# Kernel tuning notes

Measured on AMD Instinct MI355X. Metric: run time of the kernel, lower is better.

The kernel has to match this reference:

```python
import jax, jax.numpy as jnp
import numpy as np

NUM_EMB = 8192
EMB_DIM = 512
SPAN = 8            # max_span == fixed_segment_size
COMMIT = 0.25
BOUND_W = 0.01


def setup_inputs() -> dict:
    key = jax.random.key(0)
    k_x, k_e, k_w = jax.random.split(key, 3)
    B, T, D = 16, 8192, EMB_DIM
    x = jax.random.normal(k_x, (B, T, D), dtype=jnp.float32)
    emb = jax.random.normal(k_e, (NUM_EMB, D), dtype=jnp.float32) * 0.02
    Wb = jax.random.normal(k_w, (D, 1), dtype=jnp.float32) * 0.02
    bb = jnp.zeros((1,), dtype=jnp.float32)
    return {"x": x, "emb": emb, "Wb": Wb, "bb": bb}


def reference(x, emb, Wb, bb):
    # Eval-mode forward of AdaptiveTemporalVQ (no gumbel sampling, no EMA update).
    B, T, D = x.shape
    # boundary predictor: Linear(D, 1) -> squeeze
    boundary_logits = (x @ Wb)[..., 0] + bb[0]                      # [B, T]
    boundaries = (jax.nn.sigmoid(boundary_logits) > 0.5).astype(x.dtype)

    num_segments = (T + SPAN - 1) // SPAN
    pad = num_segments * SPAN - T
    x_p = jnp.pad(x, ((0, 0), (0, pad), (0, 0))) if pad > 0 else x
    # temporal mean pooling over fixed segments
    pooled = x_p.reshape(B, num_segments, SPAN, D).mean(axis=2)      # [B, S, D]

    # --- VectorQuantizer ---
    flat = pooled.reshape(-1, D)                                     # [N, D]
    dist = (jnp.sum(flat ** 2, axis=1, keepdims=True)
            + jnp.sum(emb ** 2, axis=1)
            - 2.0 * flat @ emb.T)                                    # [N, K]
    idx = jnp.argmin(dist, axis=1)                                   # [N]
    quantized = emb[idx].reshape(B, num_segments, D)                 # codebook gather

    e_latent_loss = jnp.mean((jax.lax.stop_gradient(quantized) - pooled) ** 2)
    vq_loss = COMMIT * e_latent_loss
    # straight-through estimator
    q_st = pooled + jax.lax.stop_gradient(quantized - pooled)

    # expand each segment code back over its SPAN timesteps
    q_exp = jnp.broadcast_to(q_st[:, :, None, :], (B, num_segments, SPAN, D))
    quantized_out = q_exp.reshape(B, num_segments * SPAN, D)[:, :T, :]
    idx_seg = idx.reshape(B, num_segments)
    idx_out = jnp.broadcast_to(idx_seg[:, :, None], (B, num_segments, SPAN))
    idx_out = idx_out.reshape(B, num_segments * SPAN)[:, :T]

    target_rate = jnp.float32(1.0 / SPAN)
    boundary_loss = (boundaries.mean() - target_rate) ** 2
    total_loss = vq_loss + BOUND_W * boundary_loss
    return quantized_out, total_loss, idx_out, boundaries
```

## Files before the change

### kernel.cpp

```cpp
#include <hip/hip_runtime.h>

#define B_    16
#define T_    8192
#define D_    512
#define K_    8192
#define S_    1024
#define N_    16384
#define NBT   131072

#define LOSS_OFF 67108864
#define IDX_OFF  67108865
#define BND_OFF  67239937

typedef __bf16 bf16x8 __attribute__((ext_vector_type(8)));
typedef float  f32x4  __attribute__((ext_vector_type(4)));

__device__ __forceinline__ unsigned int fsort(float f){
  unsigned int u = __float_as_uint(f);
  return (u & 0x80000000u) ? ~u : (u | 0x80000000u);
}
__device__ __forceinline__ float funsort(unsigned int su){
  unsigned int u = (su & 0x80000000u) ? (su ^ 0x80000000u) : ~su;
  return __uint_as_float(u);
}
__device__ __forceinline__ unsigned short f2bf(float f){
  unsigned int u = __float_as_uint(f);
  return (unsigned short)((u + 0x7fffu + ((u >> 16) & 1u)) >> 16);
}
__device__ __forceinline__ void gload16(const void* g, void* l){
  __builtin_amdgcn_global_load_lds((const __attribute__((address_space(1))) void*)g,
                                   (__attribute__((address_space(3))) void*)l, 16, 0, 0);
}

__global__ void k_init(int* cnt){
  if(threadIdx.x == 0 && blockIdx.x == 0) *cnt = 0;
}

__global__ void k_embnorm(const float4* __restrict__ emb4, float* __restrict__ enorm,
                          unsigned short* __restrict__ embh){
  const int wid  = (blockIdx.x * blockDim.x + threadIdx.x) >> 6;
  const int lane = threadIdx.x & 63;
  float4 a = emb4[wid * 128 + (lane << 1)];
  float4 b = emb4[wid * 128 + (lane << 1) + 1];
  float s = a.x*a.x + a.y*a.y + a.z*a.z + a.w*a.w
          + b.x*b.x + b.y*b.y + b.z*b.z + b.w*b.w;
  #pragma unroll
  for(int off = 32; off; off >>= 1) s += __shfl_xor(s, off);
  if(lane == 0) enorm[wid] = s;
  unsigned short* dst = embh + ((size_t)wid << 9) + (lane << 3);
  *(ushort4*)(dst)     = make_ushort4(f2bf(a.x), f2bf(a.y), f2bf(a.z), f2bf(a.w));
  *(ushort4*)(dst + 4) = make_ushort4(f2bf(b.x), f2bf(b.y), f2bf(b.z), f2bf(b.w));
}

__global__ void k_boundary(const float4* __restrict__ x4, const float4* __restrict__ wb4,
                           const float* __restrict__ bb, float* __restrict__ bnd,
                           int* __restrict__ cnt){
  const int lane = threadIdx.x & 63, wv = threadIdx.x >> 6;
  const int wg = (blockIdx.x << 2) + wv;
  const float4 w0 = wb4[lane << 1], w1 = wb4[(lane << 1) + 1];
  const double bbv = (double)bb[0];
  int c = 0;
  const int rbase = wg << 5;
  for(int r = 0; r < 32; r++){
    const int row = rbase + r;
    float4 a = x4[row * 128 + (lane << 1)];
    float4 b = x4[row * 128 + (lane << 1) + 1];
    double s = (double)a.x*w0.x + (double)a.y*w0.y + (double)a.z*w0.z + (double)a.w*w0.w
             + (double)b.x*w1.x + (double)b.y*w1.y + (double)b.z*w1.z + (double)b.w*w1.w;
    #pragma unroll
    for(int off = 32; off; off >>= 1) s += __shfl_xor(s, off);
    const bool f = (s + bbv) > 0.0;
    if(lane == 0){ bnd[row] = f ? 1.0f : 0.0f; c += (int)f; }
  }
  __shared__ int sc[4];
  if(lane == 0) sc[wv] = c;
  __syncthreads();
  if(threadIdx.x == 0) atomicAdd(cnt, sc[0] + sc[1] + sc[2] + sc[3]);
}

__global__ void k_pool(const float4* __restrict__ x4, float4* __restrict__ pooled4,
                       unsigned short* __restrict__ pooledh){
  const int u = blockIdx.x * 256 + threadIdx.x;
  const int row = u >> 7, c4 = u & 127;
  const int b = row >> 10, s = row & 1023;
  const float4* src = x4 + ((size_t)(b * T_ + (s << 3)) * 128 + c4);
  float4 acc = src[0];
  #pragma unroll
  for(int t = 1; t < 8; t++){
    float4 v = src[(size_t)t * 128];
    acc.x += v.x; acc.y += v.y; acc.z += v.z; acc.w += v.w;
  }
  acc.x *= 0.125f; acc.y *= 0.125f; acc.z *= 0.125f; acc.w *= 0.125f;
  pooled4[u] = acc;
  *(ushort4*)(pooledh + ((size_t)u << 2)) =
      make_ushort4(f2bf(acc.x), f2bf(acc.y), f2bf(acc.z), f2bf(acc.w));
}

__launch_bounds__(256, 2)
__global__ void k_distx(const unsigned short* __restrict__ Ah,
                        const unsigned short* __restrict__ Bh,
                        const float* __restrict__ enorm,
                        unsigned int* __restrict__ cand){
  __shared__ __align__(16) unsigned short sA[4096];
  __shared__ __align__(16) unsigned short sB[4096];
  const int tid  = threadIdx.x;
  const int w    = tid >> 6, lane = tid & 63;
  const int wm   = w >> 1,  wn   = w & 1;
  const int c    = lane & 15, q  = lane >> 4;

  const int bid   = blockIdx.x;
  const int st    = bid >> 9;
  const int loc   = bid & 511;
  const int row_t = (st << 3) + (loc & 7);
  const int col_t = loc >> 3;
  const int rowbase = row_t << 7;
  const int colbase = col_t << 7;

  f32x4 acc[4][4];
  #pragma unroll
  for(int i = 0; i < 4; i++)
    #pragma unroll
    for(int j = 0; j < 4; j++) acc[i][j] = (f32x4){0.f, 0.f, 0.f, 0.f};

  const int sr  = lane >> 2;
  const int skc = (lane & 3) << 3;

  const unsigned short* Ap0 = Ah + (size_t)(rowbase + w*32 + sr)      * 512 + skc;
  const unsigned short* Ap1 = Ah + (size_t)(rowbase + w*32 + 16 + sr) * 512 + skc;
  const unsigned short* Bp0 = Bh + (size_t)(colbase + w*32 + sr)      * 512 + skc;
  const unsigned short* Bp1 = Bh + (size_t)(colbase + w*32 + 16 + sr) * 512 + skc;
  unsigned short* lA0 = &sA[(w*32)      * 32];
  unsigned short* lA1 = &sA[(w*32 + 16) * 32];
  unsigned short* lB0 = &sB[(w*32)      * 32];
  unsigned short* lB1 = &sB[(w*32 + 16) * 32];

  for(int kb = 0; kb < 512; kb += 32){
    gload16(Ap0 + kb, lA0);
    gload16(Ap1 + kb, lA1);
    gload16(Bp0 + kb, lB0);
    gload16(Bp1 + kb, lB1);
    __syncthreads();
    bf16x8 af[4], bg[4];
    #pragma unroll
    for(int i = 0; i < 4; i++) af[i] = *(const bf16x8*)&sA[(wm*64 + i*16 + c)*32 + q*8];
    #pragma unroll
    for(int j = 0; j < 4; j++) bg[j] = *(const bf16x8*)&sB[(wn*64 + j*16 + c)*32 + q*8];
    #pragma unroll
    for(int i = 0; i < 4; i++)
      #pragma unroll
      for(int j = 0; j < 4; j++)
        acc[i][j] = __builtin_amdgcn_mfma_f32_16x16x32_bf16(af[i], bg[j], acc[i][j], 0, 0, 0);
    __syncthreads();
  }

  float en[4];
  #pragma unroll
  for(int j = 0; j < 4; j++) en[j] = enorm[colbase + wn*64 + j*16 + c];

  #pragma unroll
  for(int i = 0; i < 4; i++){
    #pragma unroll
    for(int r = 0; r < 4; r++){
      unsigned int k1 = 0xffffffffu, k2 = 0xffffffffu;
      #pragma unroll
      for(int j = 0; j < 4; j++){
        const float d = fmaf(-2.0f, acc[i][j][r], en[j]);
        const unsigned int col = (unsigned int)(colbase + wn*64 + j*16 + c);
        const unsigned int key = (fsort(d) & 0xffffe000u) | col;
        if(key < k1){ k2 = k1; k1 = key; } else if(key < k2){ k2 = key; }
      }
      #pragma unroll
      for(int off = 1; off < 16; off <<= 1){
        const unsigned int o1 = __shfl_xor(k1, off);
        const unsigned int o2 = __shfl_xor(k2, off);
        if(o1 < k1){ k2 = min(k1, o2); k1 = o1; }
        else       { k2 = min(k2, o1); }
      }
      if(c == 0){
        const int row = rowbase + wm*64 + i*16 + (q << 2) + r;
        unsigned int* o = cand + (((size_t)row << 8) + (col_t << 2) + (wn << 1));
        o[0] = k1; o[1] = k2;
      }
    }
  }
}

__launch_bounds__(256)
__global__ void k_fixup(const float* __restrict__ pooled, const float* __restrict__ emb,
                        const unsigned int* __restrict__ cand,
                        int* __restrict__ idxf, double* __restrict__ part){
  const int lane = threadIdx.x & 63, wv = threadIdx.x >> 6;
  const int row = (blockIdx.x << 2) + wv;
  const unsigned int* cr = cand + ((size_t)row << 8);
  unsigned int ks[4];
  ks[0] = cr[lane]; ks[1] = cr[lane + 64]; ks[2] = cr[lane + 128]; ks[3] = cr[lane + 192];
  unsigned int mn = min(min(ks[0], ks[1]), min(ks[2], ks[3]));
  #pragma unroll
  for(int off = 32; off; off >>= 1) mn = min(mn, (unsigned int)__shfl_xor(mn, off));
  const float thr = funsort(mn & 0xffffe000u) + 0.01f;

  double bestd = 1e300; int besti = 0x7fffffff;
  const float4* p4 = (const float4*)(pooled + ((size_t)row << 9));
  const float4 pa = p4[lane << 1], pb = p4[(lane << 1) + 1];
  #pragma unroll
  for(int g = 0; g < 4; g++){
    const bool flag = funsort(ks[g] & 0xffffe000u) <= thr;
    unsigned long long mask = __ballot(flag);
    while(mask){
      const int l = __ffsll(mask) - 1;
      mask &= mask - 1;
      const int code = (int)(__shfl(ks[g], l) & 0x1fffu);
      const float4* e4 = (const float4*)(emb + ((size_t)code << 9));
      const float4 ea = e4[lane << 1], eb = e4[(lane << 1) + 1];
      double s = 0.0, d;
      d = (double)pa.x - ea.x; s += d * d;  d = (double)pa.y - ea.y; s += d * d;
      d = (double)pa.z - ea.z; s += d * d;  d = (double)pa.w - ea.w; s += d * d;
      d = (double)pb.x - eb.x; s += d * d;  d = (double)pb.y - eb.y; s += d * d;
      d = (double)pb.z - eb.z; s += d * d;  d = (double)pb.w - eb.w; s += d * d;
      #pragma unroll
      for(int off = 32; off; off >>= 1) s += __shfl_xor(s, off);
      if(s < bestd || (s == bestd && code < besti)){ bestd = s; besti = code; }
    }
  }
  __shared__ double se[4];
  if(lane == 0){ idxf[row] = besti; se[wv] = bestd; }
  __syncthreads();
  if(threadIdx.x == 0) part[blockIdx.x] = se[0] + se[1] + se[2] + se[3];
}

__global__ void k_loss(const double* __restrict__ part, const int* __restrict__ cnt,
                       float* __restrict__ out_loss){
  const int tid = threadIdx.x;
  double s = 0.0;
  for(int i = tid; i < 4096; i += 256) s += part[i];
  #pragma unroll
  for(int off = 32; off; off >>= 1) s += __shfl_xor(s, off);
  __shared__ double sb[4];
  if((tid & 63) == 0) sb[tid >> 6] = s;
  __syncthreads();
  if(tid == 0){
    const double e  = sb[0] + sb[1] + sb[2] + sb[3];
    const double el = e / (double)((size_t)N_ * 512);
    const double bm = (double)(*cnt) / 131072.0 - 0.125;
    const double loss = 0.25 * el + 0.01 * bm * bm;
    *out_loss = (float)loss;
  }
}

__global__ void k_expand(const float4* __restrict__ emb4, const int* __restrict__ idxf,
                         float4* __restrict__ q4, float* __restrict__ idxo){
  const int u = blockIdx.x * 256 + threadIdx.x;
  const int rt = u >> 7, c4 = u & 127;
  const int seg = rt >> 3;
  const int idx = idxf[seg];
  q4[u] = emb4[idx * 128 + c4];
  if(c4 == 0) idxo[rt] = (float)idx;
}

extern "C" void kernel_launch(void* const* d_in, const int* in_sizes, int n_in,
                              void* d_out, int out_size, void* d_ws, size_t ws_size,
                              hipStream_t stream){
  const float* x   = (const float*)d_in[0];
  const float* emb = (const float*)d_in[1];
  const float* wb  = (const float*)d_in[2];
  const float* bb  = (const float*)d_in[3];
  float* out = (float*)d_out;

  char* ws = (char*)d_ws;
  int*    cnt   = (int*)(ws + 0);
  double* part  = (double*)(ws + 64);
  float*  enorm = (float*)(ws + 32832);
  int*    idxf  = (int*)(ws + 65600);

  float*          pooled  = (float*)d_out;
  unsigned int*   cand    = (unsigned int*)((char*)d_out + (48ull  << 20));
  unsigned short* pooledh = (unsigned short*)((char*)d_out + (80ull << 20));
  unsigned short* embh    = (unsigned short*)((char*)d_out + (100ull<< 20));

  float* bnd   = out + BND_OFF;
  float* idxo  = out + IDX_OFF;
  float* lossp = out + LOSS_OFF;

  hipLaunchKernelGGL(k_init,     dim3(1),     dim3(64),  0, stream, cnt);
  hipLaunchKernelGGL(k_embnorm,  dim3(2048),  dim3(256), 0, stream, (const float4*)emb, enorm, embh);
  hipLaunchKernelGGL(k_boundary, dim3(1024),  dim3(256), 0, stream, (const float4*)x, (const float4*)wb, bb, bnd, cnt);
  hipLaunchKernelGGL(k_pool,     dim3(8192),  dim3(256), 0, stream, (const float4*)x, (float4*)pooled, pooledh);
  hipLaunchKernelGGL(k_distx,    dim3(8192),  dim3(256), 0, stream, pooledh, embh, enorm, cand);
  hipLaunchKernelGGL(k_fixup,    dim3(4096),  dim3(256), 0, stream, pooled, emb, cand, idxf, part);
  hipLaunchKernelGGL(k_loss,     dim3(1),     dim3(256), 0, stream, part, cnt, lossp);
  hipLaunchKernelGGL(k_expand,   dim3(65536), dim3(256), 0, stream, (const float4*)emb, idxf, (float4*)d_out, idxo);
}
```

Before: 750.3 us.

## Fuse boundary and pooling passes, widen candidate lists, restructure expand

Merges the boundary-logit kernel and the segment-pooling kernel into one pass, so x (256 MB) is read once instead of twice. The double-precision dot products are reduced through shuffles and shared memory. The distance kernel now keeps top-2 candidates per group of 4 columns instead of per 16 and runs at higher occupancy via launch bounds. The fixup kernel then scans four times more candidates. The expand kernel loads each codebook row once per segment and writes it eight times, and workspace offsets move to fit the larger candidate buffer.

```diff
diff --git a/kernel.cpp b/kernel.cpp
--- a/kernel.cpp
+++ b/kernel.cpp
@@ -52,55 +52,64 @@
   *(ushort4*)(dst + 4) = make_ushort4(f2bf(b.x), f2bf(b.y), f2bf(b.z), f2bf(b.w));
 }
 
-__global__ void k_boundary(const float4* __restrict__ x4, const float4* __restrict__ wb4,
-                           const float* __restrict__ bb, float* __restrict__ bnd,
-                           int* __restrict__ cnt){
-  const int lane = threadIdx.x & 63, wv = threadIdx.x >> 6;
-  const int wg = (blockIdx.x << 2) + wv;
-  const float4 w0 = wb4[lane << 1], w1 = wb4[(lane << 1) + 1];
+__launch_bounds__(256)
+__global__ void k_prep(const float4* __restrict__ x4, const float4* __restrict__ wb4,
+                       const float* __restrict__ bb, float4* __restrict__ pooled4,
+                       unsigned short* __restrict__ pooledh, float* __restrict__ bnd,
+                       int* __restrict__ cnt){
+  __shared__ double ld[4][8][8];
+  const int tid  = threadIdx.x;
+  const int row0 = blockIdx.x << 5;
   const double bbv = (double)bb[0];
-  int c = 0;
-  const int rbase = wg << 5;
-  for(int r = 0; r < 32; r++){
-    const int row = rbase + r;
-    float4 a = x4[row * 128 + (lane << 1)];
-    float4 b = x4[row * 128 + (lane << 1) + 1];
-    double s = (double)a.x*w0.x + (double)a.y*w0.y + (double)a.z*w0.z + (double)a.w*w0.w
-             + (double)b.x*w1.x + (double)b.y*w1.y + (double)b.z*w1.z + (double)b.w*w1.w;
-    #pragma unroll
-    for(int off = 32; off; off >>= 1) s += __shfl_xor(s, off);
-    const bool f = (s + bbv) > 0.0;
-    if(lane == 0){ bnd[row] = f ? 1.0f : 0.0f; c += (int)f; }
-  }
-  __shared__ int sc[4];
-  if(lane == 0) sc[wv] = c;
+  #pragma unroll
+  for(int it = 0; it < 2; it++){
+    const int slot  = (it << 8) + tid;
+    const int seg_l = slot >> 7;
+    const int c4    = slot & 127;
+    const float4 w  = wb4[c4];
+    const float4* src = x4 + ((size_t)(row0 + (seg_l << 3)) * 128 + c4);
+    float4 acc = src[0];
+    double p[8];
+    p[0] = (double)acc.x*w.x + (double)acc.y*w.y + (double)acc.z*w.z + (double)acc.w*w.w;
+    #pragma unroll
+    for(int t = 1; t < 8; t++){
+      const float4 v = src[(size_t)t * 128];
+      acc.x += v.x; acc.y += v.y; acc.z += v.z; acc.w += v.w;
+      p[t] = (double)v.x*w.x + (double)v.y*w.y + (double)v.z*w.z + (double)v.w*w.w;
+    }
+    acc.x *= 0.125f; acc.y *= 0.125f; acc.z *= 0.125f; acc.w *= 0.125f;
+    const int u = ((blockIdx.x << 2) + seg_l) * 128 + c4;
+    pooled4[u] = acc;
+    *(ushort4*)(pooledh + ((size_t)u << 2)) =
+        make_ushort4(f2bf(acc.x), f2bf(acc.y), f2bf(acc.z), f2bf(acc.w));
+    #pragma unroll
+    for(int t = 0; t < 8; t++){
+      #pragma unroll
+      for(int off = 1; off < 16; off <<= 1) p[t] += __shfl_xor(p[t], off);
+    }
+    if((c4 & 15) == 0){
+      #pragma unroll
+      for(int t = 0; t < 8; t++) ld[seg_l][t][c4 >> 4] = p[t];
+    }
+  }
   __syncthreads();
-  if(threadIdx.x == 0) atomicAdd(cnt, sc[0] + sc[1] + sc[2] + sc[3]);
-}
-
-__global__ void k_pool(const float4* __restrict__ x4, float4* __restrict__ pooled4,
-                       unsigned short* __restrict__ pooledh){
-  const int u = blockIdx.x * 256 + threadIdx.x;
-  const int row = u >> 7, c4 = u & 127;
-  const int b = row >> 10, s = row & 1023;
-  const float4* src = x4 + ((size_t)(b * T_ + (s << 3)) * 128 + c4);
-  float4 acc = src[0];
-  #pragma unroll
-  for(int t = 1; t < 8; t++){
-    float4 v = src[(size_t)t * 128];
-    acc.x += v.x; acc.y += v.y; acc.z += v.z; acc.w += v.w;
-  }
-  acc.x *= 0.125f; acc.y *= 0.125f; acc.z *= 0.125f; acc.w *= 0.125f;
-  pooled4[u] = acc;
-  *(ushort4*)(pooledh + ((size_t)u << 2)) =
-      make_ushort4(f2bf(acc.x), f2bf(acc.y), f2bf(acc.z), f2bf(acc.w));
-}
-
-__launch_bounds__(256, 2)
+  if(tid < 32){
+    const double* q = ld[tid >> 3][tid & 7];
+    double s = bbv;
+    #pragma unroll
+    for(int h = 0; h < 8; h++) s += q[h];
+    const bool f = s > 0.0;
+    bnd[row0 + tid] = f ? 1.0f : 0.0f;
+    const unsigned long long m = __ballot(f);
+    if(tid == 0) atomicAdd(cnt, (int)__popcll(m));
+  }
+}
+
+__launch_bounds__(256, 4)
 __global__ void k_distx(const unsigned short* __restrict__ Ah,
                         const unsigned short* __restrict__ Bh,
                         const float* __restrict__ enorm,
-                        unsigned int* __restrict__ cand){
+                        unsigned long long* __restrict__ cand64){
   __shared__ __align__(16) unsigned short sA[4096];
   __shared__ __align__(16) unsigned short sB[4096];
   const int tid  = threadIdx.x;
@@ -170,16 +179,16 @@
         if(key < k1){ k2 = k1; k1 = key; } else if(key < k2){ k2 = key; }
       }
       #pragma unroll
-      for(int off = 1; off < 16; off <<= 1){
+      for(int off = 1; off < 4; off <<= 1){
         const unsigned int o1 = __shfl_xor(k1, off);
         const unsigned int o2 = __shfl_xor(k2, off);
         if(o1 < k1){ k2 = min(k1, o2); k1 = o1; }
         else       { k2 = min(k2, o1); }
       }
-      if(c == 0){
+      if((c & 3) == 0){
         const int row = rowbase + wm*64 + i*16 + (q << 2) + r;
-        unsigned int* o = cand + (((size_t)row << 8) + (col_t << 2) + (wn << 1));
-        o[0] = k1; o[1] = k2;
+        const int g   = (col_t << 3) + (wn << 2) + (c >> 2);
+        cand64[(size_t)row * 512 + g] = ((unsigned long long)k2 << 32) | k1;
       }
     }
   }
@@ -191,10 +200,16 @@
                         int* __restrict__ idxf, double* __restrict__ part){
   const int lane = threadIdx.x & 63, wv = threadIdx.x >> 6;
   const int row = (blockIdx.x << 2) + wv;
-  const unsigned int* cr = cand + ((size_t)row << 8);
-  unsigned int ks[4];
-  ks[0] = cr[lane]; ks[1] = cr[lane + 64]; ks[2] = cr[lane + 128]; ks[3] = cr[lane + 192];
-  unsigned int mn = min(min(ks[0], ks[1]), min(ks[2], ks[3]));
+  const uint4* cr = (const uint4*)(cand + ((size_t)row << 10));
+  unsigned int ks[16];
+  #pragma unroll
+  for(int m = 0; m < 4; m++){
+    const uint4 v = cr[m*64 + lane];
+    ks[m*4+0] = v.x; ks[m*4+1] = v.y; ks[m*4+2] = v.z; ks[m*4+3] = v.w;
+  }
+  unsigned int mn = 0xffffffffu;
+  #pragma unroll
+  for(int g = 0; g < 16; g++) mn = min(mn, ks[g]);
   #pragma unroll
   for(int off = 32; off; off >>= 1) mn = min(mn, (unsigned int)__shfl_xor(mn, off));
   const float thr = funsort(mn & 0xffffe000u) + 0.01f;
@@ -203,7 +218,7 @@
   const float4* p4 = (const float4*)(pooled + ((size_t)row << 9));
   const float4 pa = p4[lane << 1], pb = p4[(lane << 1) + 1];
   #pragma unroll
-  for(int g = 0; g < 4; g++){
+  for(int g = 0; g < 16; g++){
     const bool flag = funsort(ks[g] & 0xffffe000u) <= thr;
     unsigned long long mask = __ballot(flag);
     while(mask){
@@ -247,14 +262,21 @@
   }
 }
 
+__launch_bounds__(256)
 __global__ void k_expand(const float4* __restrict__ emb4, const int* __restrict__ idxf,
                          float4* __restrict__ q4, float* __restrict__ idxo){
-  const int u = blockIdx.x * 256 + threadIdx.x;
-  const int rt = u >> 7, c4 = u & 127;
-  const int seg = rt >> 3;
+  const int lane = threadIdx.x & 63, wv = threadIdx.x >> 6;
+  const int seg = (blockIdx.x << 2) + wv;
   const int idx = idxf[seg];
-  q4[u] = emb4[idx * 128 + c4];
-  if(c4 == 0) idxo[rt] = (float)idx;
+  const float4 a = emb4[idx * 128 + (lane << 1)];
+  const float4 b = emb4[idx * 128 + (lane << 1) + 1];
+  float4* dst = q4 + ((size_t)seg << 10);
+  #pragma unroll
+  for(int t = 0; t < 8; t++){
+    dst[t * 128 + (lane << 1)]     = a;
+    dst[t * 128 + (lane << 1) + 1] = b;
+  }
+  if(lane < 8) idxo[(seg << 3) + lane] = (float)idx;
 }
 
 extern "C" void kernel_launch(void* const* d_in, const int* in_sizes, int n_in,
@@ -272,21 +294,21 @@
   float*  enorm = (float*)(ws + 32832);
   int*    idxf  = (int*)(ws + 65600);
 
-  float*          pooled  = (float*)d_out;
-  unsigned int*   cand    = (unsigned int*)((char*)d_out + (48ull  << 20));
-  unsigned short* pooledh = (unsigned short*)((char*)d_out + (80ull << 20));
-  unsigned short* embh    = (unsigned short*)((char*)d_out + (100ull<< 20));
+  float*              pooled  = (float*)d_out;
+  unsigned long long* cand64  = (unsigned long long*)((char*)d_out + (48ull  << 20));
+  unsigned short*     pooledh = (unsigned short*)((char*)d_out + (112ull << 20));
+  unsigned short*     embh    = (unsigned short*)((char*)d_out + (128ull << 20));
 
   float* bnd   = out + BND_OFF;
   float* idxo  = out + IDX_OFF;
   float* lossp = out + LOSS_OFF;
 
-  hipLaunchKernelGGL(k_init,     dim3(1),     dim3(64),  0, stream, cnt);
-  hipLaunchKernelGGL(k_embnorm,  dim3(2048),  dim3(256), 0, stream, (const float4*)emb, enorm, embh);
-  hipLaunchKernelGGL(k_boundary, dim3(1024),  dim3(256), 0, stream, (const float4*)x, (const float4*)wb, bb, bnd, cnt);
-  hipLaunchKernelGGL(k_pool,     dim3(8192),  dim3(256), 0, stream, (const float4*)x, (float4*)pooled, pooledh);
-  hipLaunchKernelGGL(k_distx,    dim3(8192),  dim3(256), 0, stream, pooledh, embh, enorm, cand);
-  hipLaunchKernelGGL(k_fixup,    dim3(4096),  dim3(256), 0, stream, pooled, emb, cand, idxf, part);
-  hipLaunchKernelGGL(k_loss,     dim3(1),     dim3(256), 0, stream, part, cnt, lossp);
-  hipLaunchKernelGGL(k_expand,   dim3(65536), dim3(256), 0, stream, (const float4*)emb, idxf, (float4*)d_out, idxo);
-}
+  hipLaunchKernelGGL(k_init,    dim3(1),     dim3(64),  0, stream, cnt);
+  hipLaunchKernelGGL(k_embnorm, dim3(2048),  dim3(256), 0, stream, (const float4*)emb, enorm, embh);
+  hipLaunchKernelGGL(k_prep,    dim3(4096),  dim3(256), 0, stream, (const float4*)x, (const float4*)wb,
+                     bb, (float4*)pooled, pooledh, bnd, cnt);
+  hipLaunchKernelGGL(k_distx,   dim3(8192),  dim3(256), 0, stream, pooledh, embh, enorm, cand64);
+  hipLaunchKernelGGL(k_fixup,   dim3(4096),  dim3(256), 0, stream, pooled, emb, (const unsigned int*)cand64, idxf, part);
+  hipLaunchKernelGGL(k_loss,    dim3(1),     dim3(256), 0, stream, part, cnt, lossp);
+  hipLaunchKernelGGL(k_expand,  dim3(4096),  dim3(256), 0, stream, (const float4*)emb, idxf, (float4*)d_out, idxo);
+}
```

Result: faster. 702.0 us (-6.4%).
